# Kernel tuning notes

Hardware: AMD Instinct MI355X
Metric: run time of the kernel (lower is better)

## Reference

```python
import jax, jax.numpy as jnp
import numpy as np

LOG2 = float(np.log(2.0))

def ssp(x):
    # shifted softplus: log(0.5*exp(x) + 0.5)
    return jax.nn.softplus(x) - LOG2


def setup_inputs() -> dict:
    B, A, N = 8, 512, 64
    n_atom, n_spatial, n_filters = 256, 128, 256
    n_ang_feat = 2 * 2 * 2 * 8 * 2  # 2*n_zetas*2*n_angular*n_zetas = 128
    key = jax.random.key(0)
    ks = jax.random.split(key, 16)
    f32 = jnp.float32
    inp = {
        'x': jax.random.normal(ks[0], (B, A, n_atom), f32),
        'r_ij': jax.random.uniform(ks[1], (B, A, N), f32) * 6.0,  # some beyond cutoff=5
        'f_ij': jax.random.normal(ks[2], (B, A, N, n_spatial), f32),
        'G_i': jax.random.normal(ks[3], (B, A, n_ang_feat), f32),
        'neighbor_mask': jnp.ones((B, A, N), f32),
        'neighbors': jax.random.randint(ks[4], (B, A, N), 0, A),
        # CFConv params: in2f (no bias), filter MLP, f2out
        'W_in2f': jax.random.normal(ks[5], (n_atom, n_filters), f32) * (n_atom ** -0.5),
        'W1': jax.random.normal(ks[6], (n_spatial, n_filters), f32) * (n_spatial ** -0.5),
        'b1': jnp.zeros((n_filters,), f32),
        'W2': jax.random.normal(ks[7], (n_filters, n_filters), f32) * (n_filters ** -0.5),
        'b2': jnp.zeros((n_filters,), f32),
        'W_f2out': jax.random.normal(ks[8], (n_filters, n_atom), f32) * (n_filters ** -0.5),
        'b_f2out': jnp.zeros((n_atom,), f32),
        # post-cfconv dense and angular dense (no bias)
        'W_dense': jax.random.normal(ks[9], (n_atom, n_atom), f32) * (n_atom ** -0.5),
        'b_dense': jnp.zeros((n_atom,), f32),
        'W_ang': jax.random.normal(ks[10], (n_ang_feat, n_atom), f32) * (n_ang_feat ** -0.5),
    }
    return inp


def reference(x, r_ij, f_ij, G_i, neighbor_mask, neighbors,
              W_in2f, W1, b1, W2, b2, W_f2out, b_f2out,
              W_dense, b_dense, W_ang):
    cutoff = 5.0
    # filter-generating MLP on distance expansion: [B,A,N,n_filters]
    W = ssp(jnp.einsum('bans,sf->banf', f_ij, W1) + b1)
    W = jnp.einsum('banf,fg->bang', W, W2) + b2
    # hard cutoff mask on distances
    C = (r_ij <= cutoff).astype(W.dtype)
    W = W * C[..., None]
    # in2f projection then neighbor gather
    xf = jnp.einsum('bad,df->baf', x, W_in2f)  # [B,A,F]
    B, A, F = xf.shape
    N = neighbors.shape[-1]
    y = jnp.take_along_axis(xf, neighbors.reshape(B, A * N, 1), axis=1)
    y = y.reshape(B, A, N, F)
    # elementwise filter, mask padded neighbors, sum-aggregate over neighbors
    y = (y * W * neighbor_mask[..., None]).sum(axis=2)  # [B,A,F]
    v_rad = jnp.einsum('baf,fd->bad', y, W_f2out) + b_f2out
    v_rad = jnp.einsum('bad,de->bae', v_rad, W_dense) + b_dense
    v_ang = jnp.einsum('bag,gd->bad', G_i, W_ang)
    return ssp(v_rad + v_ang)
```

## Files before the change

kernel.cpp:

```cpp
#include <hip/hip_runtime.h>


typedef __bf16 bf16x8 __attribute__((ext_vector_type(8)));
typedef __bf16 bf16x2 __attribute__((ext_vector_type(2)));
typedef float f32x4 __attribute__((ext_vector_type(4)));
typedef int i32x4 __attribute__((ext_vector_type(4)));
typedef unsigned short u16;
typedef unsigned int u32;

#define LDA 136
#define LDH 264

static __device__ __forceinline__ float b2f(u16 u) {
  union { float f; u32 i; } v; v.i = ((u32)u) << 16; return v.f;
}
static __device__ __forceinline__ float b2f_lo(u32 p) {
  union { float f; u32 i; } v; v.i = p << 16; return v.f;
}
static __device__ __forceinline__ float b2f_hi(u32 p) {
  union { float f; u32 i; } v; v.i = p & 0xffff0000u; return v.f;
}
static __device__ __forceinline__ u16 f2b(float f) {
  return __builtin_bit_cast(u16, (__bf16)f);
}
static __device__ __forceinline__ u32 pk2(float lo, float hi) {
  bf16x2 v; v[0] = (__bf16)lo; v[1] = (__bf16)hi;
  return __builtin_bit_cast(u32, v);
}
static __device__ __forceinline__ float sspf(float x) {
  float t = __expf(fminf(x, 60.0f));
  return __logf(fmaf(t, 0.5f, 0.5f));
}
static __device__ __forceinline__ bf16x8 ldfrag(const u16* p) {
  return __builtin_bit_cast(bf16x8, *(const uint4*)p);
}
static __device__ __forceinline__ float ldsc(const u16* p, bool fm, size_t i) {
  return fm ? ((const float*)p)[i] : b2f(p[i]);
}

static __device__ __forceinline__ void pack_strip(
    const u16* __restrict__ W, bool fm, int q, int KC, u16* __restrict__ dst, u16* T) {
  int tid = threadIdx.x;
  if (fm) {
    const float* src = (const float*)W + (size_t)q * 32 * 256;
#pragma unroll
    for (int i = 0; i < 8; i++) {
      int c = tid + 256 * i;
      int row = c >> 6, col4 = (c & 63) * 4;
      float4 v = *(const float4*)(src + (size_t)row * 256 + col4);
      uint2 o; o.x = pk2(v.x, v.y); o.y = pk2(v.z, v.w);
      *(uint2*)(T + row * LDH + col4) = o;
    }
  } else {
    const u16* src = W + (size_t)q * 32 * 256;
#pragma unroll
    for (int i = 0; i < 8; i++) {
      int c = tid + 256 * i;
      int row = c >> 6, col4 = (c & 63) * 4;
      *(uint2*)(T + row * LDH + col4) = *(const uint2*)(src + (size_t)row * 256 + col4);
    }
  }
  __syncthreads();
#pragma unroll
  for (int i = 0; i < 4; i++) {
    int idx = tid + 256 * i;
    int flane = idx & 63, c = idx >> 6;
    int col = (c >> 2) * 64 + (flane & 15) * 4 + (c & 3);
    int r0 = (flane >> 4) * 8;
    u32 t0 = (u32)T[(r0 + 0) * LDH + col] | ((u32)T[(r0 + 1) * LDH + col] << 16);
    u32 t1 = (u32)T[(r0 + 2) * LDH + col] | ((u32)T[(r0 + 3) * LDH + col] << 16);
    u32 t2 = (u32)T[(r0 + 4) * LDH + col] | ((u32)T[(r0 + 5) * LDH + col] << 16);
    u32 t3 = (u32)T[(r0 + 6) * LDH + col] | ((u32)T[(r0 + 7) * LDH + col] << 16);
    uint4 o; o.x = t0; o.y = t1; o.z = t2; o.w = t3;
    *(uint4*)(dst + ((size_t)(c * KC + q) * 64 + flane) * 8) = o;
  }
}

__global__ __launch_bounds__(256) void pack_a(
    const u16* __restrict__ Win, const u16* __restrict__ W1, const u16* __restrict__ W2,
    const u16* __restrict__ nm, u16* __restrict__ outb) {
  __shared__ __align__(16) u16 T[32 * LDH];
  bool fm = (nm[0] == 0);
  int b = blockIdx.x;
  if (b < 8)       pack_strip(Win, fm, b,      8, outb + 1048576, T);
  else if (b < 12) pack_strip(W1,  fm, b - 8,  4, outb + 1114112, T);
  else             pack_strip(W2,  fm, b - 12, 8, outb + 1146880, T);
}

__global__ __launch_bounds__(256) void pack_b(
    const u16* __restrict__ Wf, const u16* __restrict__ Wd, const u16* __restrict__ Wa,
    const u16* __restrict__ nm, u16* __restrict__ dst) {
  __shared__ __align__(16) u16 T[32 * LDH];
  bool fm = (nm[0] == 0);
  int b = blockIdx.x;
  if (b < 8)       pack_strip(Wf, fm, b,      8, dst + 98304,  T);
  else if (b < 16) pack_strip(Wd, fm, b - 8,  8, dst + 163840, T);
  else             pack_strip(Wa, fm, b - 16, 4, dst + 229376, T);
}

__global__ __launch_bounds__(256) void k1_xf(
    const u16* __restrict__ x, const u16* __restrict__ nm, u16* __restrict__ outb) {
  __shared__ __align__(16) u16 sX[16 * LDH];
  bool fm = (nm[0] == 0);
  int bid = blockIdx.x, tid = threadIdx.x;
  int w = tid >> 6, lane = tid & 63, quad = lane >> 4, l16 = lane & 15;
  if (fm) {
    const float* src = (const float*)x + (size_t)bid * 2048;
    int c = tid;
    float4 a = *(const float4*)(src + c * 8), b = *(const float4*)(src + c * 8 + 4);
    uint4 o; o.x = pk2(a.x, a.y); o.y = pk2(a.z, a.w);
    o.z = pk2(b.x, b.y); o.w = pk2(b.z, b.w);
    *(uint4*)(sX + (c >> 5) * LDH + (c & 31) * 8) = o;
  } else {
    const u16* src = x + (size_t)bid * 2048;
    int c = tid;
    *(uint4*)(sX + (c >> 5) * LDH + (c & 31) * 8) = *(const uint4*)(src + c * 8);
  }
  __syncthreads();
  const u16* winp = outb + 1048576;
  f32x4 acc[4];
#pragma unroll
  for (int ct = 0; ct < 4; ct++) acc[ct] = (f32x4){0.f, 0.f, 0.f, 0.f};
#pragma unroll
  for (int q = 0; q < 8; q++) {
    bf16x8 af = ldfrag(sX + l16 * LDH + q * 32 + quad * 8);
    bf16x8 bfr[4];
#pragma unroll
    for (int ct = 0; ct < 4; ct++)
      bfr[ct] = ldfrag(winp + ((size_t)((w * 4 + ct) * 8 + q) * 64 + lane) * 8);
#pragma unroll
    for (int ct = 0; ct < 4; ct++)
      acc[ct] = __builtin_amdgcn_mfma_f32_16x16x32_bf16(af, bfr[ct], acc[ct], 0, 0, 0);
  }
  if (quad < 2) {
#pragma unroll
    for (int r = 0; r < 4; r++) {
      uint2 o; o.x = pk2(acc[0][r], acc[1][r]); o.y = pk2(acc[2][r], acc[3][r]);
      *(uint2*)(outb + (size_t)(bid * 8 + quad * 4 + r) * 256 + w * 64 + l16 * 4) = o;
    }
  }
}

__global__ __launch_bounds__(256, 4) void k2_main(
    u16* __restrict__ fij, const u16* __restrict__ rij, const u16* __restrict__ nm,
    const int* __restrict__ nbr, const u16* __restrict__ b1, const u16* __restrict__ b2,
    const u16* __restrict__ outb) {
  __shared__ __align__(16) u16 sU[64 * LDH];
  __shared__ __align__(16) float cm[64];
  __shared__ __align__(16) int nb[64];
  u16* sF = sU;
  u16* sH = sU;
  bool fm = (nm[0] == 0);
  const u16* xf  = outb;
  const u16* w1p = outb + 1114112;
  const u16* w2p = outb + 1146880;
  int bid = blockIdx.x, tid = threadIdx.x;
  int w = tid >> 6, lane = tid & 63, quad = lane >> 4, l16 = lane & 15;

  if (fm) {
    const float* fsrc = (const float*)fij + (size_t)bid * 8192;
#pragma unroll
    for (int i = 0; i < 4; i++) {
      int c = tid + 256 * i;
      const float* p = fsrc + c * 8;
      float4 a = *(const float4*)p, b = *(const float4*)(p + 4);
      uint4 o; o.x = pk2(a.x, a.y); o.y = pk2(a.z, a.w);
      o.z = pk2(b.x, b.y); o.w = pk2(b.z, b.w);
      *(uint4*)(sF + (c >> 4) * LDA + (c & 15) * 8) = o;
    }
  } else {
    const u16* fsrc = fij + (size_t)bid * 8192;
#pragma unroll
    for (int i = 0; i < 4; i++) {
      int c = tid + 256 * i;
      *(uint4*)(sF + (c >> 4) * LDA + (c & 15) * 8) = *(const uint4*)(fsrc + c * 8);
    }
  }
  if (tid < 64) {
    float r = ldsc(rij, fm, (size_t)bid * 64 + tid);
    float m = ldsc(nm, fm, (size_t)bid * 64 + tid);
    cm[tid] = (r <= 5.0f) ? m : 0.0f;
    nb[tid] = nbr[bid * 64 + tid];
  }
  __syncthreads();

  f32x4 zero = {0.f, 0.f, 0.f, 0.f};
  f32x4 acc[4][4];
#pragma unroll
  for (int mt = 0; mt < 4; mt++)
#pragma unroll
    for (int ct = 0; ct < 4; ct++) acc[mt][ct] = zero;
#pragma unroll
  for (int q = 0; q < 4; q++) {
    bf16x8 af[4], bfr[4];
#pragma unroll
    for (int mt = 0; mt < 4; mt++)
      af[mt] = ldfrag(sF + (mt * 16 + l16) * LDA + q * 32 + quad * 8);
#pragma unroll
    for (int ct = 0; ct < 4; ct++)
      bfr[ct] = ldfrag(w1p + ((size_t)((w * 4 + ct) * 4 + q) * 64 + lane) * 8);
#pragma unroll
    for (int mt = 0; mt < 4; mt++)
#pragma unroll
      for (int ct = 0; ct < 4; ct++)
        acc[mt][ct] = __builtin_amdgcn_mfma_f32_16x16x32_bf16(af[mt], bfr[ct], acc[mt][ct], 0, 0, 0);
  }
  __syncthreads();

  float bb1[4];
  if (fm) {
    float4 t = *(const float4*)((const float*)b1 + w * 64 + l16 * 4);
    bb1[0] = t.x; bb1[1] = t.y; bb1[2] = t.z; bb1[3] = t.w;
  } else {
    uint2 t = *(const uint2*)(b1 + w * 64 + l16 * 4);
    bb1[0] = b2f_lo(t.x); bb1[1] = b2f_hi(t.x); bb1[2] = b2f_lo(t.y); bb1[3] = b2f_hi(t.y);
  }
#pragma unroll
  for (int mt = 0; mt < 4; mt++)
#pragma unroll
    for (int r = 0; r < 4; r++) {
      int m = mt * 16 + quad * 4 + r;
      uint2 o;
      o.x = pk2(sspf(acc[mt][0][r] + bb1[0]), sspf(acc[mt][1][r] + bb1[1]));
      o.y = pk2(sspf(acc[mt][2][r] + bb1[2]), sspf(acc[mt][3][r] + bb1[3]));
      *(uint2*)(sH + m * LDH + w * 64 + l16 * 4) = o;
    }
  __syncthreads();

  f32x4 acc2[4][4];
#pragma unroll
  for (int mt = 0; mt < 4; mt++)
#pragma unroll
    for (int ct = 0; ct < 4; ct++) acc2[mt][ct] = zero;
#pragma unroll 2
  for (int q = 0; q < 8; q++) {
    bf16x8 af[4], bfr[4];
#pragma unroll
    for (int mt = 0; mt < 4; mt++)
      af[mt] = ldfrag(sH + (mt * 16 + l16) * LDH + q * 32 + quad * 8);
#pragma unroll
    for (int ct = 0; ct < 4; ct++)
      bfr[ct] = ldfrag(w2p + ((size_t)((w * 4 + ct) * 8 + q) * 64 + lane) * 8);
#pragma unroll
    for (int mt = 0; mt < 4; mt++)
#pragma unroll
      for (int ct = 0; ct < 4; ct++)
        acc2[mt][ct] = __builtin_amdgcn_mfma_f32_16x16x32_bf16(af[mt], bfr[ct], acc2[mt][ct], 0, 0, 0);
  }

  float bb2[4];
  if (fm) {
    float4 t = *(const float4*)((const float*)b2 + w * 64 + l16 * 4);
    bb2[0] = t.x; bb2[1] = t.y; bb2[2] = t.z; bb2[3] = t.w;
  } else {
    uint2 t = *(const uint2*)(b2 + w * 64 + l16 * 4);
    bb2[0] = b2f_lo(t.x); bb2[1] = b2f_hi(t.x); bb2[2] = b2f_lo(t.y); bb2[3] = b2f_hi(t.y);
  }
  int b_of = (bid >> 9) * 512;
  const u16* xcol = xf + w * 64 + l16 * 4;
  float s0 = 0.f, s1 = 0.f, s2 = 0.f, s3 = 0.f;
#pragma unroll
  for (int mt = 0; mt < 4; mt++) {
    f32x4 cmv = *(const f32x4*)(cm + mt * 16 + quad * 4);
    i32x4 nbv = *(const i32x4*)(nb + mt * 16 + quad * 4);
#pragma unroll
    for (int r = 0; r < 4; r++) {
      uint2 xv = *(const uint2*)(xcol + (size_t)(b_of + nbv[r]) * 256);
      float c = cmv[r];
      s0 = fmaf((acc2[mt][0][r] + bb2[0]) * c, b2f_lo(xv.x), s0);
      s1 = fmaf((acc2[mt][1][r] + bb2[1]) * c, b2f_hi(xv.x), s1);
      s2 = fmaf((acc2[mt][2][r] + bb2[2]) * c, b2f_lo(xv.y), s2);
      s3 = fmaf((acc2[mt][3][r] + bb2[3]) * c, b2f_hi(xv.y), s3);
    }
  }
  s0 += __shfl_xor(s0, 16); s0 += __shfl_xor(s0, 32);
  s1 += __shfl_xor(s1, 16); s1 += __shfl_xor(s1, 32);
  s2 += __shfl_xor(s2, 16); s2 += __shfl_xor(s2, 32);
  s3 += __shfl_xor(s3, 16); s3 += __shfl_xor(s3, 32);
  if (quad == 0) {
    size_t yoff = (size_t)bid * (fm ? 16384 : 8192);
    uint2 o; o.x = pk2(s0, s1); o.y = pk2(s2, s3);
    *(uint2*)(fij + yoff + w * 64 + l16 * 4) = o;
  }
}

__global__ __launch_bounds__(512) void k3_out(
    const u16* __restrict__ fij, const u16* __restrict__ G, const u16* __restrict__ bf2,
    const u16* __restrict__ bd, const u16* __restrict__ nm,
    const u16* __restrict__ packed, u16* __restrict__ outb) {
  __shared__ __align__(16) u16 sY[16 * LDH];
  __shared__ __align__(16) u16 sH2[16 * LDH];
  __shared__ __align__(16) u16 sG[16 * LDA];
  bool fm = (nm[0] == 0);
  const u16* wfp = packed + 98304;
  const u16* wdp = packed + 163840;
  const u16* wap = packed + 229376;
  int bid = blockIdx.x, tid = threadIdx.x;
  int cg = tid >> 6, lane = tid & 63, quad = lane >> 4, l16 = lane & 15;
  int f0 = (cg >> 1) * 64 + l16 * 4 + (cg & 1) * 2;
  size_t ystr = fm ? 16384 : 8192;
  {
    int c = tid;
    const u16* src = fij + (size_t)(bid * 16 + (c >> 5)) * ystr + (c & 31) * 8;
    *(uint4*)(sY + (c >> 5) * LDH + (c & 31) * 8) = *(const uint4*)src;
  }
  if (fm) {
    if (tid < 256) {
      int c = tid;
      const float* p = (const float*)G + (size_t)(bid * 16 + (c >> 4)) * 128 + (c & 15) * 8;
      float4 a = *(const float4*)p, b = *(const float4*)(p + 4);
      uint4 o; o.x = pk2(a.x, a.y); o.y = pk2(a.z, a.w);
      o.z = pk2(b.x, b.y); o.w = pk2(b.z, b.w);
      *(uint4*)(sG + (c >> 4) * LDA + (c & 15) * 8) = o;
    }
  } else {
    if (tid < 256) {
      int c = tid;
      *(uint4*)(sG + (c >> 4) * LDA + (c & 15) * 8) =
          *(const uint4*)(G + (size_t)(bid * 16 + (c >> 4)) * 128 + (c & 15) * 8);
    }
  }
  __syncthreads();
  f32x4 zero = {0.f, 0.f, 0.f, 0.f};
  f32x4 acc[2];
  acc[0] = zero; acc[1] = zero;
#pragma unroll
  for (int q = 0; q < 8; q++) {
    bf16x8 af = ldfrag(sY + l16 * LDH + q * 32 + quad * 8);
    bf16x8 bfr[2];
#pragma unroll
    for (int ct = 0; ct < 2; ct++)
      bfr[ct] = ldfrag(wfp + ((size_t)((cg * 2 + ct) * 8 + q) * 64 + lane) * 8);
#pragma unroll
    for (int ct = 0; ct < 2; ct++)
      acc[ct] = __builtin_amdgcn_mfma_f32_16x16x32_bf16(af, bfr[ct], acc[ct], 0, 0, 0);
  }
  float bm0, bm1;
  if (fm) {
    float2 t = *(const float2*)((const float*)bf2 + f0);
    bm0 = t.x; bm1 = t.y;
  } else {
    u32 t = *(const u32*)(bf2 + f0);
    bm0 = b2f_lo(t); bm1 = b2f_hi(t);
  }
#pragma unroll
  for (int r = 0; r < 4; r++) {
    int m = quad * 4 + r;
    *(u32*)(sH2 + m * LDH + f0) = pk2(acc[0][r] + bm0, acc[1][r] + bm1);
  }
  __syncthreads();
  acc[0] = zero; acc[1] = zero;
#pragma unroll
  for (int q = 0; q < 8; q++) {
    bf16x8 af = ldfrag(sH2 + l16 * LDH + q * 32 + quad * 8);
    bf16x8 bfr[2];
#pragma unroll
    for (int ct = 0; ct < 2; ct++)
      bfr[ct] = ldfrag(wdp + ((size_t)((cg * 2 + ct) * 8 + q) * 64 + lane) * 8);
#pragma unroll
    for (int ct = 0; ct < 2; ct++)
      acc[ct] = __builtin_amdgcn_mfma_f32_16x16x32_bf16(af, bfr[ct], acc[ct], 0, 0, 0);
  }
#pragma unroll
  for (int q = 0; q < 4; q++) {
    bf16x8 af = ldfrag(sG + l16 * LDA + q * 32 + quad * 8);
    bf16x8 bfr[2];
#pragma unroll
    for (int ct = 0; ct < 2; ct++)
      bfr[ct] = ldfrag(wap + ((size_t)((cg * 2 + ct) * 4 + q) * 64 + lane) * 8);
#pragma unroll
    for (int ct = 0; ct < 2; ct++)
      acc[ct] = __builtin_amdgcn_mfma_f32_16x16x32_bf16(af, bfr[ct], acc[ct], 0, 0, 0);
  }
  float bd0, bd1;
  if (fm) {
    float2 t = *(const float2*)((const float*)bd + f0);
    bd0 = t.x; bd1 = t.y;
  } else {
    u32 t = *(const u32*)(bd + f0);
    bd0 = b2f_lo(t); bd1 = b2f_hi(t);
  }
  float* out32 = (float*)outb;
#pragma unroll
  for (int r = 0; r < 4; r++) {
    size_t row = (size_t)bid * 16 + quad * 4 + r;
    float v0 = sspf(acc[0][r] + bd0);
    float v1 = sspf(acc[1][r] + bd1);
    if (fm) {
      float2 o; o.x = v0; o.y = v1;
      *(float2*)(out32 + row * 256 + f0) = o;
    } else {
      *(u32*)(outb + row * 256 + f0) = pk2(v0, v1);
    }
  }
}

extern "C" void kernel_launch(void* const* d_in, const int* in_sizes, int n_in,
                              void* d_out, int out_size, void* d_ws, size_t ws_size,
                              hipStream_t stream) {
  u16*       x    = (u16*)d_in[0];
  const u16* rij  = (const u16*)d_in[1];
  u16*       fij  = (u16*)d_in[2];
  const u16* Gi   = (const u16*)d_in[3];
  const u16* nmsk = (const u16*)d_in[4];
  const int* nbr  = (const int*)d_in[5];
  const u16* Win  = (const u16*)d_in[6];
  const u16* W1   = (const u16*)d_in[7];
  const u16* b1   = (const u16*)d_in[8];
  const u16* W2   = (const u16*)d_in[9];
  const u16* b2   = (const u16*)d_in[10];
  const u16* Wf   = (const u16*)d_in[11];
  const u16* bf2  = (const u16*)d_in[12];
  const u16* Wd   = (const u16*)d_in[13];
  const u16* bd   = (const u16*)d_in[14];
  const u16* Wa   = (const u16*)d_in[15];
  u16* out = (u16*)d_out;

  pack_a<<<20, 256, 0, stream>>>(Win, W1, W2, nmsk, out);
  k1_xf<<<512, 256, 0, stream>>>(x, nmsk, out);
  pack_b<<<20, 256, 0, stream>>>(Wf, Wd, Wa, nmsk, x);
  k2_main<<<4096, 256, 0, stream>>>(fij, rij, nmsk, nbr, b1, b2, out);
  k3_out<<<256, 512, 0, stream>>>(fij, Gi, bf2, bd, nmsk, x, out);
}
```

Before: 287.7 us.

## Prefetch neighbor gathers early in k2, split LDS buffers, use workspace scratch

The main kernel now issues the neighbor-indexed xf gathers and cutoff-mask loads into registers at kernel start, so their latency overlaps the f_ij staging and both MFMA GEMMs instead of sitting at the end. It gives sF and sH separate LDS buffers, which removes one barrier but raises LDS use, so occupancy is lowered to 3 blocks and the second GEMM loop is fully unrolled. When a workspace is available it merges the weight packing into one launch and writes the intermediate y to scratch rather than back into the input buffers. The costs are higher register pressure and lower occupancy.

Measured after the change: 310.7 us. +8.0%, slower.

```diff
diff --git a/kernel.cpp b/kernel.cpp
--- a/kernel.cpp
+++ b/kernel.cpp
@@ -11,6 +11,19 @@
 #define LDA 136
 #define LDH 264
 
+#define O_WIN 1048576
+#define O_W1  1114112
+#define O_W2  1146880
+#define O_WF  1212416
+#define O_WD  1277952
+#define O_WA  1343488
+#define O_Y   1376256
+#define WS_NEED ((size_t)(2424832) * 2)
+
+#define X_WF 98304
+#define X_WD 163840
+#define X_WA 229376
+
 static __device__ __forceinline__ float b2f(u16 u) {
   union { float f; u32 i; } v; v.i = ((u32)u) << 16; return v.f;
 }
@@ -19,9 +32,6 @@
 }
 static __device__ __forceinline__ float b2f_hi(u32 p) {
   union { float f; u32 i; } v; v.i = p & 0xffff0000u; return v.f;
-}
-static __device__ __forceinline__ u16 f2b(float f) {
-  return __builtin_bit_cast(u16, (__bf16)f);
 }
 static __device__ __forceinline__ u32 pk2(float lo, float hi) {
   bf16x2 v; v[0] = (__bf16)lo; v[1] = (__bf16)hi;
@@ -76,15 +86,30 @@
   }
 }
 
+__global__ __launch_bounds__(256) void pack6(
+    const u16* __restrict__ Win, const u16* __restrict__ W1, const u16* __restrict__ W2,
+    const u16* __restrict__ Wf, const u16* __restrict__ Wd, const u16* __restrict__ Wa,
+    const u16* __restrict__ nm, u16* __restrict__ base) {
+  __shared__ __align__(16) u16 T[32 * LDH];
+  bool fm = (nm[0] == 0);
+  int b = blockIdx.x;
+  if (b < 8)       pack_strip(Win, fm, b,      8, base + O_WIN, T);
+  else if (b < 12) pack_strip(W1,  fm, b - 8,  4, base + O_W1,  T);
+  else if (b < 20) pack_strip(W2,  fm, b - 12, 8, base + O_W2,  T);
+  else if (b < 28) pack_strip(Wf,  fm, b - 20, 8, base + O_WF,  T);
+  else if (b < 36) pack_strip(Wd,  fm, b - 28, 8, base + O_WD,  T);
+  else             pack_strip(Wa,  fm, b - 36, 4, base + O_WA,  T);
+}
+
 __global__ __launch_bounds__(256) void pack_a(
     const u16* __restrict__ Win, const u16* __restrict__ W1, const u16* __restrict__ W2,
     const u16* __restrict__ nm, u16* __restrict__ outb) {
   __shared__ __align__(16) u16 T[32 * LDH];
   bool fm = (nm[0] == 0);
   int b = blockIdx.x;
-  if (b < 8)       pack_strip(Win, fm, b,      8, outb + 1048576, T);
-  else if (b < 12) pack_strip(W1,  fm, b - 8,  4, outb + 1114112, T);
-  else             pack_strip(W2,  fm, b - 12, 8, outb + 1146880, T);
+  if (b < 8)       pack_strip(Win, fm, b,      8, outb + O_WIN, T);
+  else if (b < 12) pack_strip(W1,  fm, b - 8,  4, outb + O_W1,  T);
+  else             pack_strip(W2,  fm, b - 12, 8, outb + O_W2,  T);
 }
 
 __global__ __launch_bounds__(256) void pack_b(
@@ -93,13 +118,14 @@
   __shared__ __align__(16) u16 T[32 * LDH];
   bool fm = (nm[0] == 0);
   int b = blockIdx.x;
-  if (b < 8)       pack_strip(Wf, fm, b,      8, dst + 98304,  T);
-  else if (b < 16) pack_strip(Wd, fm, b - 8,  8, dst + 163840, T);
-  else             pack_strip(Wa, fm, b - 16, 4, dst + 229376, T);
+  if (b < 8)       pack_strip(Wf, fm, b,      8, dst + X_WF, T);
+  else if (b < 16) pack_strip(Wd, fm, b - 8,  8, dst + X_WD, T);
+  else             pack_strip(Wa, fm, b - 16, 4, dst + X_WA, T);
 }
 
 __global__ __launch_bounds__(256) void k1_xf(
-    const u16* __restrict__ x, const u16* __restrict__ nm, u16* __restrict__ outb) {
+    const u16* __restrict__ x, const u16* __restrict__ nm,
+    const u16* __restrict__ winp, u16* __restrict__ xfout) {
   __shared__ __align__(16) u16 sX[16 * LDH];
   bool fm = (nm[0] == 0);
   int bid = blockIdx.x, tid = threadIdx.x;
@@ -117,7 +143,6 @@
     *(uint4*)(sX + (c >> 5) * LDH + (c & 31) * 8) = *(const uint4*)(src + c * 8);
   }
   __syncthreads();
-  const u16* winp = outb + 1048576;
   f32x4 acc[4];
 #pragma unroll
   for (int ct = 0; ct < 4; ct++) acc[ct] = (f32x4){0.f, 0.f, 0.f, 0.f};
@@ -136,26 +161,48 @@
 #pragma unroll
     for (int r = 0; r < 4; r++) {
       uint2 o; o.x = pk2(acc[0][r], acc[1][r]); o.y = pk2(acc[2][r], acc[3][r]);
-      *(uint2*)(outb + (size_t)(bid * 8 + quad * 4 + r) * 256 + w * 64 + l16 * 4) = o;
-    }
-  }
-}
-
-__global__ __launch_bounds__(256, 4) void k2_main(
-    u16* __restrict__ fij, const u16* __restrict__ rij, const u16* __restrict__ nm,
+      *(uint2*)(xfout + (size_t)(bid * 8 + quad * 4 + r) * 256 + w * 64 + l16 * 4) = o;
+    }
+  }
+}
+
+__global__ __launch_bounds__(256, 3) void k2_main(
+    const u16* __restrict__ fij, const u16* __restrict__ rij, const u16* __restrict__ nm,
     const int* __restrict__ nbr, const u16* __restrict__ b1, const u16* __restrict__ b2,
-    const u16* __restrict__ outb) {
-  __shared__ __align__(16) u16 sU[64 * LDH];
-  __shared__ __align__(16) float cm[64];
-  __shared__ __align__(16) int nb[64];
-  u16* sF = sU;
-  u16* sH = sU;
-  bool fm = (nm[0] == 0);
-  const u16* xf  = outb;
-  const u16* w1p = outb + 1114112;
-  const u16* w2p = outb + 1146880;
+    const u16* __restrict__ xf, const u16* __restrict__ w1p, const u16* __restrict__ w2p,
+    u16* __restrict__ yout, int ystr) {
+  __shared__ __align__(16) u16 sF[64 * LDA];
+  __shared__ __align__(16) u16 sH[64 * LDH];
+  bool fm = (nm[0] == 0);
   int bid = blockIdx.x, tid = threadIdx.x;
   int w = tid >> 6, lane = tid & 63, quad = lane >> 4, l16 = lane & 15;
+
+  float cmv[4][4];
+  uint2 xv[4][4];
+  {
+    const u16* xcol = xf + (size_t)((bid >> 9) * 512) * 256 + w * 64 + l16 * 4;
+#pragma unroll
+    for (int mt = 0; mt < 4; mt++) {
+      int mb = bid * 64 + mt * 16 + quad * 4;
+      i32x4 nbv = *(const i32x4*)(nbr + mb);
+      if (fm) {
+        f32x4 rv = *(const f32x4*)((const float*)rij + mb);
+        f32x4 mv = *(const f32x4*)((const float*)nm + mb);
+#pragma unroll
+        for (int r = 0; r < 4; r++) cmv[mt][r] = (rv[r] <= 5.0f) ? mv[r] : 0.0f;
+      } else {
+        uint2 rv = *(const uint2*)(rij + mb);
+        uint2 mv = *(const uint2*)(nm + mb);
+        cmv[mt][0] = (b2f_lo(rv.x) <= 5.0f) ? b2f_lo(mv.x) : 0.0f;
+        cmv[mt][1] = (b2f_hi(rv.x) <= 5.0f) ? b2f_hi(mv.x) : 0.0f;
+        cmv[mt][2] = (b2f_lo(rv.y) <= 5.0f) ? b2f_lo(mv.y) : 0.0f;
+        cmv[mt][3] = (b2f_hi(rv.y) <= 5.0f) ? b2f_hi(mv.y) : 0.0f;
+      }
+#pragma unroll
+      for (int r = 0; r < 4; r++)
+        xv[mt][r] = *(const uint2*)(xcol + (size_t)nbv[r] * 256);
+    }
+  }
 
   if (fm) {
     const float* fsrc = (const float*)fij + (size_t)bid * 8192;
@@ -176,12 +223,6 @@
       *(uint4*)(sF + (c >> 4) * LDA + (c & 15) * 8) = *(const uint4*)(fsrc + c * 8);
     }
   }
-  if (tid < 64) {
-    float r = ldsc(rij, fm, (size_t)bid * 64 + tid);
-    float m = ldsc(nm, fm, (size_t)bid * 64 + tid);
-    cm[tid] = (r <= 5.0f) ? m : 0.0f;
-    nb[tid] = nbr[bid * 64 + tid];
-  }
   __syncthreads();
 
   f32x4 zero = {0.f, 0.f, 0.f, 0.f};
@@ -205,7 +246,6 @@
       for (int ct = 0; ct < 4; ct++)
         acc[mt][ct] = __builtin_amdgcn_mfma_f32_16x16x32_bf16(af[mt], bfr[ct], acc[mt][ct], 0, 0, 0);
   }
-  __syncthreads();
 
   float bb1[4];
   if (fm) {
@@ -232,7 +272,7 @@
   for (int mt = 0; mt < 4; mt++)
 #pragma unroll
     for (int ct = 0; ct < 4; ct++) acc2[mt][ct] = zero;
-#pragma unroll 2
+#pragma unroll
   for (int q = 0; q < 8; q++) {
     bf16x8 af[4], bfr[4];
 #pragma unroll
@@ -256,21 +296,17 @@
     uint2 t = *(const uint2*)(b2 + w * 64 + l16 * 4);
     bb2[0] = b2f_lo(t.x); bb2[1] = b2f_hi(t.x); bb2[2] = b2f_lo(t.y); bb2[3] = b2f_hi(t.y);
   }
-  int b_of = (bid >> 9) * 512;
-  const u16* xcol = xf + w * 64 + l16 * 4;
   float s0 = 0.f, s1 = 0.f, s2 = 0.f, s3 = 0.f;
 #pragma unroll
   for (int mt = 0; mt < 4; mt++) {
-    f32x4 cmv = *(const f32x4*)(cm + mt * 16 + quad * 4);
-    i32x4 nbv = *(const i32x4*)(nb + mt * 16 + quad * 4);
 #pragma unroll
     for (int r = 0; r < 4; r++) {
-      uint2 xv = *(const uint2*)(xcol + (size_t)(b_of + nbv[r]) * 256);
-      float c = cmv[r];
-      s0 = fmaf((acc2[mt][0][r] + bb2[0]) * c, b2f_lo(xv.x), s0);
-      s1 = fmaf((acc2[mt][1][r] + bb2[1]) * c, b2f_hi(xv.x), s1);
-      s2 = fmaf((acc2[mt][2][r] + bb2[2]) * c, b2f_lo(xv.y), s2);
-      s3 = fmaf((acc2[mt][3][r] + bb2[3]) * c, b2f_hi(xv.y), s3);
+      uint2 v = xv[mt][r];
+      float c = cmv[mt][r];
+      s0 = fmaf((acc2[mt][0][r] + bb2[0]) * c, b2f_lo(v.x), s0);
+      s1 = fmaf((acc2[mt][1][r] + bb2[1]) * c, b2f_hi(v.x), s1);
+      s2 = fmaf((acc2[mt][2][r] + bb2[2]) * c, b2f_lo(v.y), s2);
+      s3 = fmaf((acc2[mt][3][r] + bb2[3]) * c, b2f_hi(v.y), s3);
     }
   }
   s0 += __shfl_xor(s0, 16); s0 += __shfl_xor(s0, 32);
@@ -278,30 +314,26 @@
   s2 += __shfl_xor(s2, 16); s2 += __shfl_xor(s2, 32);
   s3 += __shfl_xor(s3, 16); s3 += __shfl_xor(s3, 32);
   if (quad == 0) {
-    size_t yoff = (size_t)bid * (fm ? 16384 : 8192);
     uint2 o; o.x = pk2(s0, s1); o.y = pk2(s2, s3);
-    *(uint2*)(fij + yoff + w * 64 + l16 * 4) = o;
+    *(uint2*)(yout + (size_t)bid * ystr + w * 64 + l16 * 4) = o;
   }
 }
 
 __global__ __launch_bounds__(512) void k3_out(
-    const u16* __restrict__ fij, const u16* __restrict__ G, const u16* __restrict__ bf2,
-    const u16* __restrict__ bd, const u16* __restrict__ nm,
-    const u16* __restrict__ packed, u16* __restrict__ outb) {
+    const u16* __restrict__ y, int ystr, const u16* __restrict__ G,
+    const u16* __restrict__ bf2, const u16* __restrict__ bd, const u16* __restrict__ nm,
+    const u16* __restrict__ wfp, const u16* __restrict__ wdp, const u16* __restrict__ wap,
+    u16* __restrict__ outb) {
   __shared__ __align__(16) u16 sY[16 * LDH];
   __shared__ __align__(16) u16 sH2[16 * LDH];
   __shared__ __align__(16) u16 sG[16 * LDA];
   bool fm = (nm[0] == 0);
-  const u16* wfp = packed + 98304;
-  const u16* wdp = packed + 163840;
-  const u16* wap = packed + 229376;
   int bid = blockIdx.x, tid = threadIdx.x;
   int cg = tid >> 6, lane = tid & 63, quad = lane >> 4, l16 = lane & 15;
   int f0 = (cg >> 1) * 64 + l16 * 4 + (cg & 1) * 2;
-  size_t ystr = fm ? 16384 : 8192;
   {
     int c = tid;
-    const u16* src = fij + (size_t)(bid * 16 + (c >> 5)) * ystr + (c & 31) * 8;
+    const u16* src = y + (size_t)(bid * 16 + (c >> 5)) * ystr + (c & 31) * 8;
     *(uint4*)(sY + (c >> 5) * LDH + (c & 31) * 8) = *(const uint4*)src;
   }
   if (fm) {
@@ -416,9 +448,25 @@
   const u16* Wa   = (const u16*)d_in[15];
   u16* out = (u16*)d_out;
 
-  pack_a<<<20, 256, 0, stream>>>(Win, W1, W2, nmsk, out);
-  k1_xf<<<512, 256, 0, stream>>>(x, nmsk, out);
-  pack_b<<<20, 256, 0, stream>>>(Wf, Wd, Wa, nmsk, x);
-  k2_main<<<4096, 256, 0, stream>>>(fij, rij, nmsk, nbr, b1, b2, out);
-  k3_out<<<256, 512, 0, stream>>>(fij, Gi, bf2, bd, nmsk, x, out);
-}
+  bool fmh = (in_sizes[1] == 8 * 512 * 64 * 4);
+  bool usews = (ws_size >= WS_NEED) && (d_ws != nullptr);
+
+  if (usews) {
+    u16* ws = (u16*)d_ws;
+    pack6<<<40, 256, 0, stream>>>(Win, W1, W2, Wf, Wd, Wa, nmsk, ws);
+    k1_xf<<<512, 256, 0, stream>>>(x, nmsk, ws + O_WIN, ws);
+    k2_main<<<4096, 256, 0, stream>>>(fij, rij, nmsk, nbr, b1, b2,
+                                      ws, ws + O_W1, ws + O_W2, ws + O_Y, 256);
+    k3_out<<<256, 512, 0, stream>>>(ws + O_Y, 256, Gi, bf2, bd, nmsk,
+                                    ws + O_WF, ws + O_WD, ws + O_WA, out);
+  } else {
+    int ystr = fmh ? 16384 : 8192;
+    pack_a<<<20, 256, 0, stream>>>(Win, W1, W2, nmsk, out);
+    k1_xf<<<512, 256, 0, stream>>>(x, nmsk, out + O_WIN, out);
+    pack_b<<<20, 256, 0, stream>>>(Wf, Wd, Wa, nmsk, x);
+    k2_main<<<4096, 256, 0, stream>>>(fij, rij, nmsk, nbr, b1, b2,
+                                      out, out + O_W1, out + O_W2, fij, ystr);
+    k3_out<<<256, 512, 0, stream>>>(fij, ystr, Gi, bf2, bd, nmsk,
+                                    x + X_WF, x + X_WD, x + X_WA, out);
+  }
+}
```
